# Optimization experiments

Measured on AMD Instinct MI355X. Metric: run time of the kernel, lower is better.

## Reference

```python
import jax, jax.numpy as jnp
import numpy as np

N = 16777216  # number of samples
G = 16        # number of distinct group ids


def setup_inputs() -> dict:
    key = jax.random.key(0)
    k1, k2, k3, k4, k5 = jax.random.split(key, 5)
    u1 = jax.random.uniform(k1, (N,), dtype=jnp.float32)
    u2 = jax.random.uniform(k2, (N,), dtype=jnp.float32)
    u3 = jax.random.uniform(k3, (N,), dtype=jnp.float32)
    u4 = jax.random.uniform(k4, (N,), dtype=jnp.float32)
    return {
        "shape": 0.5 + 1.0 * u1,              # Weibull shape b in [0.5, 1.5]
        "scale": 0.8 + 1.2 * u2,              # Weibull scale a in [0.8, 2.0]
        "time": 0.1 + 2.9 * u3,               # survival time y in [0.1, 3.0]
        "event": (u4 > 0.5).astype(jnp.float32),  # event indicator u in {0,1}
        "lengths": jnp.arange(N, dtype=jnp.int32),   # only len(lengths)=N is used
        "group": jax.random.randint(k5, (N,), 0, G, dtype=jnp.int32),
    }


def reference(shape, scale, time, event, lengths, group):
    b, a, y, u = shape, scale, time, event
    # Per-sample Weibull NLL (torch.mean over a scalar is identity).
    hazard0 = (y + 1e-35 / a) ** b
    hazard1 = (y + 1.0 / a) ** b
    per_sample = -(u * jnp.log(jnp.exp(hazard1 - hazard0) - 1.0) - hazard1)  # [N]
    # Overall loss: sum / len(lengths) == mean over samples.
    loss = jnp.mean(per_sample)
    # Per-group mean via segment-sum (dict accumulation in the original).
    ones = jnp.ones_like(per_sample)
    counts = jax.ops.segment_sum(ones, group, num_segments=G)         # [G]
    gsum = jax.ops.segment_sum(per_sample, group, num_segments=G)     # [G]
    group_losses = gsum / jnp.maximum(counts, 1.0)                    # [G]
    return loss, group_losses
```

## Files before the change

### kernel.cpp

```cpp
#include <hip/hip_runtime.h>


namespace {
constexpr int NG = 16;
constexpr int BLOCK = 256;
constexpr int ST  = NG + 1;
constexpr int CST = 20;
constexpr int GRID = 1792;
constexpr float LOG2E = 1.4426950408889634f;
constexpr float LN2   = 0.6931471805599453f;
}

typedef float f32x4 __attribute__((ext_vector_type(4)));
typedef int   i32x4 __attribute__((ext_vector_type(4)));

__device__ __forceinline__ float flog2(float x) { return __builtin_amdgcn_logf(x); }
__device__ __forceinline__ float fexp2(float x) { return __builtin_amdgcn_exp2f(x); }
__device__ __forceinline__ float frcp(float x)  { return __builtin_amdgcn_rcpf(x); }

__device__ __forceinline__ float per_sample(float b, float a, float y, float u) {
    const float inva = frcp(a);
    const float h1 = fexp2(b * flog2(y + inva));
    const float h0 = fexp2(b * flog2(y));
    const float em1 = fexp2((h1 - h0) * LOG2E) - 1.0f;
    const float t = flog2(em1) * LN2;
    return __builtin_fmaf(-u, t, h1);
}

struct Grp { f32x4 b, a, y, u; i32x4 g; };

__global__ __launch_bounds__(BLOCK, 4) void gssl_main_kernel(
    const float* __restrict__ bptr,
    const float* __restrict__ aptr,
    const float* __restrict__ yptr,
    const float* __restrict__ uptr,
    const int*   __restrict__ gptr,
    float* __restrict__ ws,
    int per_block, int n4, int n)
{
    __shared__ float lsum[BLOCK * ST];
    __shared__ unsigned char lcnt8[BLOCK * CST];
    __shared__ float sbin[2 * NG];
    const int tid = threadIdx.x;
    const int myrow = tid * ST;
    const int mycrow = tid * CST;

    #pragma unroll
    for (int q = 0; q < ST; ++q) lsum[myrow + q] = 0.0f;
    #pragma unroll
    for (int q = 0; q < CST; ++q) lcnt8[mycrow + q] = 0;
    if (tid < 2 * NG) sbin[tid] = 0.0f;

    const int base = blockIdx.x * per_block;
    const int rem  = n4 - base;
    const int jend = (rem < per_block) ? (rem < 0 ? 0 : rem) : per_block;

    auto ld = [&](int i) {
        Grp r;
        r.b = __builtin_nontemporal_load(reinterpret_cast<const f32x4*>(bptr) + i);
        r.a = __builtin_nontemporal_load(reinterpret_cast<const f32x4*>(aptr) + i);
        r.y = __builtin_nontemporal_load(reinterpret_cast<const f32x4*>(yptr) + i);
        r.u = __builtin_nontemporal_load(reinterpret_cast<const f32x4*>(uptr) + i);
        r.g = __builtin_nontemporal_load(reinterpret_cast<const i32x4*>(gptr) + i);
        return r;
    };

    auto do4 = [&](const Grp& G) {
        #pragma unroll
        for (int k = 0; k < 4; ++k) {
            const float ps = per_sample(G.b[k], G.a[k], G.y[k], G.u[k]);
            const int g = G.g[k];
            lsum[myrow + g] += ps;
            lcnt8[mycrow + g] += 1;
        }
    };

    int j = tid;
    if (j + BLOCK < jend) {
        Grp a0 = ld(base + j);
        Grp b0 = ld(base + j + BLOCK);
        j += 2 * BLOCK;
        while (j + BLOCK < jend) {
            Grp a1 = ld(base + j);
            Grp b1 = ld(base + j + BLOCK);
            __builtin_amdgcn_sched_barrier(0);
            do4(a0);
            do4(b0);
            a0 = a1; b0 = b1;
            j += 2 * BLOCK;
        }
        do4(a0);
        do4(b0);
    }
    for (; j < jend; j += BLOCK) do4(ld(base + j));

    __syncthreads();

    const int q = tid & 15, c = tid >> 4;
    float s = 0.0f, cnt = 0.0f;
    #pragma unroll
    for (int r = 0; r < 16; ++r) {
        const int row = c * 16 + r;
        s   += lsum[row * ST + q];
        cnt += (float)lcnt8[row * CST + q];
    }
    s   += __shfl_xor(s, 16, 64);   s   += __shfl_xor(s, 32, 64);
    cnt += __shfl_xor(cnt, 16, 64); cnt += __shfl_xor(cnt, 32, 64);
    if ((tid & 48) == 0) {
        atomicAdd(&sbin[q], s);
        atomicAdd(&sbin[NG + q], cnt);
    }
    __syncthreads();

    if (tid < 2 * NG) atomicAdd(&ws[tid], sbin[tid]);

    if (blockIdx.x == 0 && tid == 0) {
        for (int i = n4 * 4; i < n; ++i) {
            const float ps = per_sample(bptr[i], aptr[i], yptr[i], uptr[i]);
            atomicAdd(&ws[gptr[i]], ps);
            atomicAdd(&ws[NG + gptr[i]], 1.0f);
        }
    }
}

__global__ __launch_bounds__(64) void gssl_final_kernel(
    const float* __restrict__ ws, float* __restrict__ out, float invN)
{
    const int t = threadIdx.x;
    if (t < NG) {
        const float gs = ws[t];
        const float gc = ws[NG + t];
        out[1 + t] = gs / fmaxf(gc, 1.0f);
    }
    float v = (t < NG) ? ws[t] : 0.0f;
    #pragma unroll
    for (int off = 32; off > 0; off >>= 1) v += __shfl_down(v, off);
    if (t == 0) out[0] = v * invN;
}

extern "C" void kernel_launch(void* const* d_in, const int* in_sizes, int n_in,
                              void* d_out, int out_size, void* d_ws, size_t ws_size,
                              hipStream_t stream) {
    const float* shape_p = (const float*)d_in[0];
    const float* scale_p = (const float*)d_in[1];
    const float* time_p  = (const float*)d_in[2];
    const float* event_p = (const float*)d_in[3];
    const int*   group_p = (const int*)d_in[5];
    float* out = (float*)d_out;
    float* ws  = (float*)d_ws;

    const int n  = in_sizes[0];
    const int n4 = n >> 2;

    (void)hipMemsetAsync(ws, 0, 2 * NG * sizeof(float), stream);

    const int per_block = (n4 + GRID - 1) / GRID;

    hipLaunchKernelGGL(gssl_main_kernel, dim3(GRID), dim3(BLOCK), 0, stream,
                       shape_p, scale_p, time_p, event_p, group_p, ws,
                       per_block, n4, n);
    hipLaunchKernelGGL(gssl_final_kernel, dim3(1), dim3(64), 0, stream,
                       ws, out, 1.0f / (float)n);
}
```

Before: 68.84 us.

## Transpose per-thread LDS histograms to group-major layout and drop shared bin stage

Changes the per-thread LDS histogram from thread-major rows with padding to a group-major layout where each group occupies a contiguous 256-slot row indexed by thread id. The lane-varying part of every LDS address is now the thread index, so a wave's scatter-adds map to distinct banks regardless of group values. The block reduction now reads one group per 16 threads, reduces with xor shuffles, and issues global atomics directly, removing the shared bin array and one barrier. The grid grows to 2048 blocks with per-block work rounded up to a multiple of 64, and an explicit barrier after LDS initialisation is added.

```diff
diff --git a/kernel.cpp b/kernel.cpp
--- a/kernel.cpp
+++ b/kernel.cpp
@@ -4,9 +4,7 @@
 namespace {
 constexpr int NG = 16;
 constexpr int BLOCK = 256;
-constexpr int ST  = NG + 1;
-constexpr int CST = 20;
-constexpr int GRID = 1792;
+constexpr int GRID = 2048;
 constexpr float LOG2E = 1.4426950408889634f;
 constexpr float LN2   = 0.6931471805599453f;
 }
@@ -38,18 +36,16 @@
     float* __restrict__ ws,
     int per_block, int n4, int n)
 {
-    __shared__ float lsum[BLOCK * ST];
-    __shared__ unsigned char lcnt8[BLOCK * CST];
-    __shared__ float sbin[2 * NG];
+    __shared__ float lsum[NG * BLOCK];
+    __shared__ unsigned char lcnt8[NG * BLOCK];
     const int tid = threadIdx.x;
-    const int myrow = tid * ST;
-    const int mycrow = tid * CST;
 
     #pragma unroll
-    for (int q = 0; q < ST; ++q) lsum[myrow + q] = 0.0f;
+    for (int r = 0; r < NG; ++r) lsum[r * BLOCK + tid] = 0.0f;
     #pragma unroll
-    for (int q = 0; q < CST; ++q) lcnt8[mycrow + q] = 0;
-    if (tid < 2 * NG) sbin[tid] = 0.0f;
+    for (int r = 0; r < NG * BLOCK / 4 / BLOCK; ++r)
+        reinterpret_cast<unsigned int*>(lcnt8)[r * BLOCK + tid] = 0u;
+    __syncthreads();
 
     const int base = blockIdx.x * per_block;
     const int rem  = n4 - base;
@@ -70,8 +66,8 @@
         for (int k = 0; k < 4; ++k) {
             const float ps = per_sample(G.b[k], G.a[k], G.y[k], G.u[k]);
             const int g = G.g[k];
-            lsum[myrow + g] += ps;
-            lcnt8[mycrow + g] += 1;
+            lsum[(g << 8) + tid] += ps;
+            lcnt8[(g << 8) + tid] += 1;
         }
     };
 
@@ -96,23 +92,23 @@
 
     __syncthreads();
 
-    const int q = tid & 15, c = tid >> 4;
+    const int q  = tid >> 4;
+    const int s0 = tid & 15;
     float s = 0.0f, cnt = 0.0f;
     #pragma unroll
     for (int r = 0; r < 16; ++r) {
-        const int row = c * 16 + r;
-        s   += lsum[row * ST + q];
-        cnt += (float)lcnt8[row * CST + q];
+        const int slot = s0 + (r << 4);
+        s   += lsum[(q << 8) + slot];
+        cnt += (float)lcnt8[(q << 8) + slot];
     }
-    s   += __shfl_xor(s, 16, 64);   s   += __shfl_xor(s, 32, 64);
-    cnt += __shfl_xor(cnt, 16, 64); cnt += __shfl_xor(cnt, 32, 64);
-    if ((tid & 48) == 0) {
-        atomicAdd(&sbin[q], s);
-        atomicAdd(&sbin[NG + q], cnt);
+    s   += __shfl_xor(s, 1, 64);   s   += __shfl_xor(s, 2, 64);
+    s   += __shfl_xor(s, 4, 64);   s   += __shfl_xor(s, 8, 64);
+    cnt += __shfl_xor(cnt, 1, 64); cnt += __shfl_xor(cnt, 2, 64);
+    cnt += __shfl_xor(cnt, 4, 64); cnt += __shfl_xor(cnt, 8, 64);
+    if (s0 == 0) {
+        atomicAdd(&ws[q], s);
+        atomicAdd(&ws[NG + q], cnt);
     }
-    __syncthreads();
-
-    if (tid < 2 * NG) atomicAdd(&ws[tid], sbin[tid]);
 
     if (blockIdx.x == 0 && tid == 0) {
         for (int i = n4 * 4; i < n; ++i) {
@@ -154,7 +150,8 @@
 
     (void)hipMemsetAsync(ws, 0, 2 * NG * sizeof(float), stream);
 
-    const int per_block = (n4 + GRID - 1) / GRID;
+    int per_block = (n4 + GRID - 1) / GRID;
+    per_block = (per_block + 63) & ~63;
 
     hipLaunchKernelGGL(gssl_main_kernel, dim3(GRID), dim3(BLOCK), 0, stream,
                        shape_p, scale_p, time_p, event_p, group_p, ws,
```

New measurement: 133.1 us. 1.93x slower.
